# Kernel optimization log

Hardware: AMD Instinct MI355X
Metric: run time of the kernel (lower is better)

The kernel has to match this reference:

```python
import jax, jax.numpy as jnp
import numpy as np
from functools import partial

B, L, V = 64, 512, 20000
P, M = 150, 6          # total patterns, max pattern length
NEG = -1e9             # semiring zero (log-space)
END_STATES = np.repeat(np.array([3, 4, 5]), 50)  # pattern_len-1 per pattern


@jax.custom_vjp
def ste_heaviside(x):
    return (x > 0).astype(x.dtype)

def _ste_fwd(x):
    return ste_heaviside(x), None

def _ste_bwd(_, g):
    return (g,)  # straight-through identity (matches torch code path)

ste_heaviside.defvjp(_ste_fwd, _ste_bwd)


def setup_inputs() -> dict:
    key = jax.random.key(0)
    ks = jax.random.split(key, 8)
    return {
        "docs": jax.random.randint(ks[0], (B, L), 0, V),
        "doc_lens": jax.random.randint(ks[1], (B,), 1, L),
        "local_embeddings": jax.random.normal(ks[2], (300, V), jnp.float32),
        "diags": jax.random.normal(ks[3], (P * M, 300), jnp.float32) * 0.05,
        "bias": jax.random.normal(ks[4], (P * M, 1), jnp.float32) * 0.05,
        "wildcards": jax.random.normal(ks[5], (P, M - 1), jnp.float32) * 0.05,
        "ln_gamma": jnp.ones((P,), jnp.float32),
        "ln_beta": jnp.zeros((P,), jnp.float32),
        "linear_w": jax.random.normal(ks[6], (2, P), jnp.float32) * 0.05,
        "linear_b": jnp.zeros((2,), jnp.float32),
    }


def reference(docs, doc_lens, local_embeddings, diags, bias, wildcards,
              ln_gamma, ln_beta, linear_w, linear_b):
    end_states = jnp.asarray(END_STATES)                  # [P]
    pat_idx = jnp.arange(P)

    # transition matrices over local vocab, mapped into log-space semiring
    tm_vocab = jax.nn.log_sigmoid((diags @ local_embeddings + bias).T)  # [V, P*M]
    tm = tm_vocab[docs].reshape(B, L, P, M)               # [B,L,P,M]

    # wildcard transitions: semiring.times(one=0, log_sigmoid(wildcards))
    wild = jax.nn.log_sigmoid(wildcards)                  # [P, M-1]

    restart = jnp.zeros((B, P, 1), tm.dtype)              # semiring one
    hid0 = jnp.full((B, P, M), NEG, tm.dtype).at[:, :, 0].set(0.0)
    scores0 = jnp.full((B, P), NEG, tm.dtype)             # semiring zero

    def step(carry, inputs):
        hid, sc = carry
        t, tm_t = inputs                                  # tm_t: [B,P,M]
        main = jnp.concatenate([restart, hid[:, :, :-1] + tm_t[:, :, :-1]], axis=2)
        wildp = jnp.concatenate([restart, hid[:, :, :-1] + wild[None]], axis=2)
        hid = jnp.maximum(main, wildp)                    # semiring plus
        esv = hid[:, pat_idx, end_states]                 # [B,P]
        active = (doc_lens > t)[:, None]
        sc = jnp.where(active, jnp.maximum(sc, esv), sc)
        return (hid, sc), None

    xs = (jnp.arange(L), jnp.moveaxis(tm, 1, 0))          # [L], [L,B,P,M]
    (_, scores), _ = jax.lax.scan(step, (hid0, scores0), xs)

    scores = jnp.exp(scores)                              # from_semiring_to_outer
    mu = scores.mean(axis=-1, keepdims=True)
    var = scores.var(axis=-1, keepdims=True)
    norm = (scores - mu) * jax.lax.rsqrt(var + 1e-5) * ln_gamma + ln_beta
    binar = ste_heaviside(norm)
    return binar @ linear_w.T + linear_b
```

## Files before the change

kernel.cpp:

```cpp
#include <hip/hip_runtime.h>
#include <hip/hip_bf16.h>
#include <hip/hip_fp16.h>
#include <math.h>

#define B_   64
#define L_   512
#define V_   20000
#define P_   150
#define M_   6
#define KDIM 300
#define NOUT 750
#define CWS  752
#define NEGF (-1.0e9f)

#define BM 128
#define BN 128
#define BK 16
#define LDP 132

#define KP 320
#define NIT 10
#define NVG 157
#define NJ  6
#define TILE_U4 1024
#define SA 1024.0f
#define SB 16384.0f
#define INV24 (5.9604644775390625e-8f)

#define TCHUNK 32
#define NCHUNK (L_ / TCHUNK)
#define WARM   5
#define CS_STRIDE 160

typedef _Float16 f16x8 __attribute__((ext_vector_type(8)));
typedef float f32x16 __attribute__((ext_vector_type(16)));

__device__ __forceinline__ float logsigf(float x) {
    return fminf(x, 0.f) - log1pf(expf(-fabsf(x)));
}

__device__ __forceinline__ float logsigf_fast(float x) {
    return fminf(x, 0.f) - __logf(1.f + __expf(-fabsf(x)));
}


__global__ __launch_bounds__(256) void p12_split(
    const float* __restrict__ emb, const float* __restrict__ diags,
    uint4* __restrict__ a_t, uint4* __restrict__ b_t)
{
    __shared__ float T[64][132];
    const int t   = threadIdx.x;
    const int bid = blockIdx.x;

    if (bid < NVG * 5) {
        const int gx = bid % NVG;
        const int ky = bid / NVG;
        const int v0 = gx * 128;
        const int k0 = ky * 64;

        #pragma unroll
        for (int pass = 0; pass < 8; ++pass) {
            int flat = pass * 256 + t;
            int krow = flat >> 5;
            int c4   = (flat & 31) * 4;
            int kg   = k0 + krow;
            int v    = v0 + c4;
            float4 f = {0.f, 0.f, 0.f, 0.f};
            if (kg < KDIM && v + 3 < V_)
                f = *(const float4*)(emb + (size_t)kg * V_ + v);
            *(float4*)&T[krow][c4] = f;
        }
        __syncthreads();

        const int vv = t >> 1;
        const int kh = (t & 1) * 32;
        const int it = ky * 2 + (kh >> 5);
        const int v  = v0 + vv;
        if (v < V_) {
            union { ushort u[8]; uint4 q; } H[4], Lo[4];
            #pragma unroll
            for (int i = 0; i < 32; ++i) {
                float x = T[kh + i][vv] * SA;
                __half h = __float2half_rn(x);
                float rem = x - __half2float(h);
                H[i >> 3].u[i & 7]  = __half_as_ushort(h);
                Lo[i >> 3].u[i & 7] = __half_as_ushort(__float2half_rn(rem));
            }
            uint4* tile = a_t + ((size_t)gx * NIT + it) * TILE_U4;
            #pragma unroll
            for (int c = 0; c < 4; ++c) {
                tile[      c * 128 + vv] = H[c].q;
                tile[512 + c * 128 + vv] = Lo[c].q;
            }
        }
    } else {
        const int bidx = bid - NVG * 5;
        const int it   = bidx % NIT;
        const int j    = bidx / NIT;
        const int row  = t >> 1;
        const int qh   = (t & 1) * 2;
        const int n    = j * 128 + row;
        const bool nok = (n < NOUT);
        const int pm   = nok ? ((n / 5) * 6 + (n % 5)) : 0;
        uint4* tile = b_t + (size_t)bidx * TILE_U4;
        #pragma unroll
        for (int qq = 0; qq < 2; ++qq) {
            int q = qh + qq;
            union { ushort u[8]; uint4 v; } H, Lo;
            #pragma unroll
            for (int e = 0; e < 8; ++e) {
                int k = it * 32 + q * 8 + e;
                float x = (nok && k < KDIM) ? diags[(size_t)pm * KDIM + k] * SB : 0.f;
                __half h = __float2half_rn(x);
                float rem = x - __half2float(h);
                H.u[e]  = __half_as_ushort(h);
                Lo.u[e] = __half_as_ushort(__float2half_rn(rem));
            }
            tile[      q * 128 + row] = H.v;
            tile[512 + q * 128 + row] = Lo.v;
        }
    }
}

__global__ __attribute__((amdgpu_waves_per_eu(4))) __launch_bounds__(256)
void k1m_gemm(
    const uint4* __restrict__ a_t, const uint4* __restrict__ b_t,
    const float* __restrict__ bias, const float* __restrict__ wildc,
    float* __restrict__ cw)
{
    const int bid  = blockIdx.x;
    const int xcd  = bid & 7;
    const int slot = bid >> 3;
    const int g    = xcd + 8 * (slot / 6);
    const int j    = slot % 6;
    if (g >= NVG) return;

    const int t    = threadIdx.x;
    const int lane = t & 63;
    const int w    = t >> 6;
    const int wr   = w >> 1, wc = w & 1;
    const int v0   = g * 128;
    const int n0   = j * 128;

    const int fk16 = lane >> 5;
    const int fm   = lane & 31;

    const uint4* abase = a_t + (size_t)g * NIT * TILE_U4;
    const uint4* bbase = b_t + (size_t)j * NIT * TILE_U4;

    f32x16 acc[2][2];
    #pragma unroll
    for (int i = 0; i < 2; ++i)
        #pragma unroll
        for (int jj = 0; jj < 2; ++jj)
            #pragma unroll
            for (int e = 0; e < 16; ++e) acc[i][jj][e] = 0.f;

    #pragma unroll
    for (int it = 0; it < NIT; ++it) {
        const uint4* atile = abase + (size_t)it * TILE_U4;
        const uint4* btile = bbase + (size_t)it * TILE_U4;
        #pragma unroll
        for (int s = 0; s < 2; ++s) {
            const int q = s * 2 + fk16;
            f16x8 A1[2], A2[2], B1[2], B2[2];
            #pragma unroll
            for (int ri = 0; ri < 2; ++ri) {
                const uint4* ap = atile + q * 128 + wr * 64 + ri * 32 + fm;
                A1[ri] = *(const f16x8*)ap;
                A2[ri] = *(const f16x8*)(ap + 512);
            }
            #pragma unroll
            for (int cj = 0; cj < 2; ++cj) {
                const uint4* bp = btile + q * 128 + wc * 64 + cj * 32 + fm;
                B1[cj] = *(const f16x8*)bp;
                B2[cj] = *(const f16x8*)(bp + 512);
            }
            #pragma unroll
            for (int ri = 0; ri < 2; ++ri)
                #pragma unroll
                for (int cj = 0; cj < 2; ++cj) {
                    acc[ri][cj] = __builtin_amdgcn_mfma_f32_32x32x16_f16(A1[ri], B1[cj], acc[ri][cj], 0, 0, 0);
                    acc[ri][cj] = __builtin_amdgcn_mfma_f32_32x32x16_f16(A1[ri], B2[cj], acc[ri][cj], 0, 0, 0);
                    acc[ri][cj] = __builtin_amdgcn_mfma_f32_32x32x16_f16(A2[ri], B1[cj], acc[ri][cj], 0, 0, 0);
                }
        }
    }

    float biasv[2], lwv[2]; int ncol[2]; bool nok[2];
    #pragma unroll
    for (int cj = 0; cj < 2; ++cj) {
        int n = n0 + wc * 64 + cj * 32 + fm;
        ncol[cj] = n;
        nok[cj]  = (n < NOUT);
        int nc = nok[cj] ? n : 0;
        int pm = (nc / 5) * 6 + (nc % 5);
        biasv[cj] = bias[pm];
        lwv[cj]   = logsigf_fast(wildc[nc]);
    }
    #pragma unroll
    for (int ri = 0; ri < 2; ++ri) {
        int vbase = v0 + wr * 64 + ri * 32 + 4 * fk16;
        #pragma unroll
        for (int cj = 0; cj < 2; ++cj) {
            if (!nok[cj]) continue;
            #pragma unroll
            for (int e = 0; e < 16; ++e) {
                int v = vbase + (e & 3) + 8 * (e >> 2);
                if (v < V_) {
                    float val = acc[ri][cj][e] * INV24 + biasv[cj];
                    cw[(size_t)v * CWS + ncol[cj]] = fmaxf(logsigf_fast(val), lwv[cj]);
                }
            }
        }
    }
}


__global__ __launch_bounds__(256) void k1_gemm_cw(
    const float* __restrict__ emb,
    const float* __restrict__ diags,
    const float* __restrict__ bias,
    const float* __restrict__ wildc,
    float* __restrict__ cw)
{
    __shared__ float As[BK][LDP];
    __shared__ float Bs[BK][LDP];

    const int tid = threadIdx.x;
    const int v0 = blockIdx.x * BM;
    const int n0 = blockIdx.y * BN;
    const int tx = tid & 15;
    const int ty = tid >> 4;

    float acc[8][8];
    #pragma unroll
    for (int i = 0; i < 8; ++i)
        #pragma unroll
        for (int j = 0; j < 8; ++j) acc[i][j] = 0.f;

    const int a_k = tid >> 4;
    const int a_v = (tid & 15) * 8;
    const int b_n   = tid >> 1;
    const int b_kof = (tid & 1) * 8;

    int  brow;
    bool bval;
    {
        int n = n0 + b_n;
        bval = (n < NOUT);
        brow = bval ? ((n / 5) * 6 + (n % 5)) : 0;
    }

    for (int k0 = 0; k0 < KDIM; k0 += BK) {
        {
            float4 f0 = {0,0,0,0}, f1 = {0,0,0,0};
            int k = k0 + a_k;
            if (k < KDIM) {
                const float* src = emb + (size_t)k * V_ + v0 + a_v;
                if (v0 + a_v + 3 < V_) f0 = *(const float4*)src;
                if (v0 + a_v + 7 < V_) f1 = *(const float4*)(src + 4);
            }
            *(float4*)&As[a_k][a_v]     = f0;
            *(float4*)&As[a_k][a_v + 4] = f1;
        }
        {
            float4 f = {0,0,0,0}, g = {0,0,0,0};
            if (bval) {
                const float* src = diags + (size_t)brow * KDIM + k0 + b_kof;
                if (k0 + b_kof + 3 < KDIM) f = *(const float4*)src;
                if (k0 + b_kof + 7 < KDIM) g = *(const float4*)(src + 4);
            }
            Bs[b_kof + 0][b_n] = f.x;
            Bs[b_kof + 1][b_n] = f.y;
            Bs[b_kof + 2][b_n] = f.z;
            Bs[b_kof + 3][b_n] = f.w;
            Bs[b_kof + 4][b_n] = g.x;
            Bs[b_kof + 5][b_n] = g.y;
            Bs[b_kof + 6][b_n] = g.z;
            Bs[b_kof + 7][b_n] = g.w;
        }
        __syncthreads();
        #pragma unroll
        for (int k = 0; k < BK; ++k) {
            float4 a0 = *(const float4*)&As[k][tx * 4];
            float4 a1 = *(const float4*)&As[k][64 + tx * 4];
            float4 b0 = *(const float4*)&Bs[k][ty * 8];
            float4 b1 = *(const float4*)&Bs[k][ty * 8 + 4];
            float av[8] = {a0.x, a0.y, a0.z, a0.w, a1.x, a1.y, a1.z, a1.w};
            float bv[8] = {b0.x, b0.y, b0.z, b0.w, b1.x, b1.y, b1.z, b1.w};
            #pragma unroll
            for (int i = 0; i < 8; ++i)
                #pragma unroll
                for (int j = 0; j < 8; ++j)
                    acc[i][j] = fmaf(av[i], bv[j], acc[i][j]);
        }
        __syncthreads();
    }

    float biasv[8], lwv[8];
    #pragma unroll
    for (int j = 0; j < 8; ++j) {
        int n  = n0 + ty * 8 + j;
        int nc = (n < NOUT) ? n : 0;
        int pm = (nc / 5) * 6 + (nc % 5);
        biasv[j] = bias[pm];
        lwv[j]   = logsigf(wildc[nc]);
    }
    #pragma unroll
    for (int i = 0; i < 8; ++i) {
        int v = v0 + ((i < 4) ? (tx * 4 + i) : (64 + tx * 4 + (i - 4)));
        if (v >= V_) continue;
        float r[8];
        #pragma unroll
        for (int j = 0; j < 8; ++j)
            r[j] = fmaxf(logsigf(acc[i][j] + biasv[j]), lwv[j]);
        float* dst = cw + (size_t)v * CWS + n0 + ty * 8;
        if (n0 + ty * 8     < NOUT) *(float4*)dst       = make_float4(r[0], r[1], r[2], r[3]);
        if (n0 + ty * 8 + 4 < NOUT) *(float4*)(dst + 4) = make_float4(r[4], r[5], r[6], r[7]);
    }
}


__global__ __launch_bounds__(192) void k2_scan(
    const int* __restrict__ docs,
    const int* __restrict__ doc_lens,
    const float* __restrict__ cw,
    float* __restrict__ cs)
{
    const int ci = blockIdx.x;
    const int b  = blockIdx.y;
    const int t0 = ci * TCHUNK;
    const int ts = (t0 >= WARM) ? (t0 - WARM) : 0;
    const int dl = doc_lens[b];
    const int te = min(t0 + TCHUNK, dl);
    const int nt = te - ts;

    __shared__ int toks[TCHUNK + WARM];

    const int t = threadIdx.x;
    if (t < TCHUNK + WARM) {
        int tt = ts + t;
        toks[t] = docs[b * L_ + min(tt, L_ - 1)];
    }
    __syncthreads();

    const int p      = t;
    const int e      = (p < 50) ? 3 : (p < 100) ? 4 : 5;
    const int warm_n = t0 - ts;
    float h1 = NEGF, h2 = NEGF, h3 = NEGF, h4 = NEGF, h5 = NEGF, sc = NEGF;

    if (p < P_ && nt > 0) {
        const size_t poff = (size_t)p * 5;
        float A0 = 0, A1 = 0, A2 = 0, A3 = 0, A4 = 0;
        float B0 = 0, B1 = 0, B2 = 0, B3 = 0, B4 = 0;
        {
            const float* r = cw + (size_t)toks[0] * CWS + poff;
            A0 = r[0]; A1 = r[1]; A2 = r[2]; A3 = r[3]; A4 = r[4];
        }
        if (nt > 1) {
            const float* r = cw + (size_t)toks[1] * CWS + poff;
            B0 = r[0]; B1 = r[1]; B2 = r[2]; B3 = r[3]; B4 = r[4];
        }
        for (int i = 0; i < nt; i += 2) {
            float c0 = A0, c1 = A1, c2 = A2, c3 = A3, c4 = A4;
            if (i + 2 < nt) {
                const float* r = cw + (size_t)toks[i + 2] * CWS + poff;
                A0 = r[0]; A1 = r[1]; A2 = r[2]; A3 = r[3]; A4 = r[4];
            }
            h5 = h4 + c4;
            h4 = h3 + c3;
            h3 = h2 + c2;
            h2 = h1 + c1;
            h1 = c0;
            if (i >= warm_n) {
                float esv = (e == 3) ? h3 : (e == 4) ? h4 : h5;
                sc = fmaxf(sc, esv);
            }
            if (i + 1 < nt) {
                float d0 = B0, d1 = B1, d2 = B2, d3 = B3, d4 = B4;
                if (i + 3 < nt) {
                    const float* r = cw + (size_t)toks[i + 3] * CWS + poff;
                    B0 = r[0]; B1 = r[1]; B2 = r[2]; B3 = r[3]; B4 = r[4];
                }
                h5 = h4 + d4;
                h4 = h3 + d3;
                h3 = h2 + d2;
                h2 = h1 + d1;
                h1 = d0;
                if (i + 1 >= warm_n) {
                    float esv = (e == 3) ? h3 : (e == 4) ? h4 : h5;
                    sc = fmaxf(sc, esv);
                }
            }
        }
    }
    if (p < P_) cs[(size_t)(b * NCHUNK + ci) * CS_STRIDE + p] = sc;
}

__device__ __forceinline__ float block_sum192(float v, volatile float* red, int tid) {
    #pragma unroll
    for (int off = 32; off > 0; off >>= 1) v += __shfl_down(v, off, 64);
    __syncthreads();
    if ((tid & 63) == 0) red[tid >> 6] = v;
    __syncthreads();
    return red[0] + red[1] + red[2];
}

__global__ __launch_bounds__(192) void k3_final(
    const float* __restrict__ cs,
    const float* __restrict__ gamma,
    const float* __restrict__ beta,
    const float* __restrict__ lw,
    const float* __restrict__ lb,
    float* __restrict__ out)
{
    __shared__ float red[3];
    const int b   = blockIdx.x;
    const int tid = threadIdx.x;
    float s = 0.f;
    if (tid < P_) {
        float m = NEGF;
        const float* row = cs + (size_t)b * NCHUNK * CS_STRIDE + tid;
        #pragma unroll
        for (int ci = 0; ci < NCHUNK; ++ci) m = fmaxf(m, row[ci * CS_STRIDE]);
        s = expf(m);
    }
    float mu = block_sum192(s, red, tid) * (1.f / P_);
    float d  = (tid < P_) ? (s - mu) : 0.f;
    float var = block_sum192(d * d, red, tid) * (1.f / P_);
    float bin = 0.f;
    if (tid < P_) {
        float norm = (s - mu) * rsqrtf(var + 1e-5f) * gamma[tid] + beta[tid];
        bin = (norm > 0.f) ? 1.f : 0.f;
    }
    float o0 = block_sum192((tid < P_) ? bin * lw[tid]      : 0.f, red, tid);
    float o1 = block_sum192((tid < P_) ? bin * lw[P_ + tid] : 0.f, red, tid);
    if (tid == 0) {
        out[b * 2 + 0] = o0 + lb[0];
        out[b * 2 + 1] = o1 + lb[1];
    }
}

extern "C" void kernel_launch(void* const* d_in, const int* in_sizes, int n_in,
                              void* d_out, int out_size, void* d_ws, size_t ws_size,
                              hipStream_t stream)
{
    const int*   docs  = (const int*)  d_in[0];
    const int*   dlens = (const int*)  d_in[1];
    const float* emb   = (const float*)d_in[2];
    const float* diags = (const float*)d_in[3];
    const float* bias  = (const float*)d_in[4];
    const float* wildc = (const float*)d_in[5];
    const float* gamma = (const float*)d_in[6];
    const float* beta  = (const float*)d_in[7];
    const float* lw    = (const float*)d_in[8];
    const float* lb    = (const float*)d_in[9];
    float* out = (float*)d_out;

    const size_t cw_b = (size_t)V_ * CWS * 4;
    const size_t cs_b = (size_t)B_ * NCHUNK * CS_STRIDE * 4;
    const size_t at_b = (size_t)NVG * NIT * TILE_U4 * 16;
    const size_t bt_b = (size_t)NJ  * NIT * TILE_U4 * 16;
    const size_t need = cw_b + cs_b + at_b + bt_b;

    char* base = (char*)d_ws;
    float* cw = (float*)base;
    float* cs = (float*)(base + cw_b);
    uint4* at = (uint4*)(base + cw_b + cs_b);
    uint4* bt = (uint4*)(base + cw_b + cs_b + at_b);

    if (ws_size >= need) {
        p12_split<<<NVG * 5 + NJ * NIT, 256, 0, stream>>>(emb, diags, at, bt);
        k1m_gemm<<<960, 256, 0, stream>>>(at, bt, bias, wildc, cw);
    } else {
        dim3 g1((V_ + BM - 1) / BM, (NOUT + BN - 1) / BN);
        k1_gemm_cw<<<g1, 256, 0, stream>>>(emb, diags, bias, wildc, cw);
    }

    dim3 g2(NCHUNK, B_);
    k2_scan<<<g2, 192, 0, stream>>>(docs, dlens, cw, cs);
    k3_final<<<B_, 192, 0, stream>>>(cs, gamma, beta, lw, lb, out);
}
```

Before: 158.8 us.

## Enlarge GEMM block and warp tiles to raise register reuse of operands

The split-fp16 MFMA GEMM now uses 512-thread blocks covering 256 vocab rows by 256 output columns. Each wave computes a 128x64 tile with 4x2 accumulators instead of 64x64, and the grid drops from 960 to 240 blocks with a new block-to-XCD mapping. Each wave gets more MFMAs per global fragment load, which cuts redundant global and cache traffic. In exchange it needs far more accumulator registers, runs at 2 waves per EU, and the last row group is clamped so it recomputes and rewrites identical values.

After: 156.8 us. About the same (-1.2%).

```diff
diff --git a/kernel.cpp b/kernel.cpp
--- a/kernel.cpp
+++ b/kernel.cpp
@@ -122,35 +122,36 @@
     }
 }
 
-__global__ __attribute__((amdgpu_waves_per_eu(4))) __launch_bounds__(256)
+__global__ __attribute__((amdgpu_waves_per_eu(2, 2))) __launch_bounds__(512)
 void k1m_gemm(
     const uint4* __restrict__ a_t, const uint4* __restrict__ b_t,
     const float* __restrict__ bias, const float* __restrict__ wildc,
     float* __restrict__ cw)
 {
-    const int bid  = blockIdx.x;
-    const int xcd  = bid & 7;
-    const int slot = bid >> 3;
-    const int g    = xcd + 8 * (slot / 6);
-    const int j    = slot % 6;
-    if (g >= NVG) return;
+    const int bid = blockIdx.x;
+    const int c   = bid / 24;
+    const int r   = bid % 24;
+    const int gp  = c * 8 + (r & 7);
+    const int h   = r >> 3;
+    if (gp >= 79) return;
 
     const int t    = threadIdx.x;
     const int lane = t & 63;
     const int w    = t >> 6;
-    const int wr   = w >> 1, wc = w & 1;
-    const int v0   = g * 128;
-    const int n0   = j * 128;
-
+    const int wr   = w >> 2;
+    const int wc   = w & 3;
     const int fk16 = lane >> 5;
     const int fm   = lane & 31;
 
-    const uint4* abase = a_t + (size_t)g * NIT * TILE_U4;
-    const uint4* bbase = b_t + (size_t)j * NIT * TILE_U4;
-
-    f32x16 acc[2][2];
-    #pragma unroll
-    for (int i = 0; i < 2; ++i)
+    const int ga = (2 * gp + wr < NVG) ? (2 * gp + wr) : (NVG - 1);
+    const uint4* abase = a_t + (size_t)ga * NIT * TILE_U4;
+    const int bg   = 2 * h + (wc >> 1);
+    const int bcol = (wc & 1) * 64;
+    const uint4* bbase = b_t + (size_t)bg * NIT * TILE_U4;
+
+    f32x16 acc[4][2];
+    #pragma unroll
+    for (int i = 0; i < 4; ++i)
         #pragma unroll
         for (int jj = 0; jj < 2; ++jj)
             #pragma unroll
@@ -163,21 +164,21 @@
         #pragma unroll
         for (int s = 0; s < 2; ++s) {
             const int q = s * 2 + fk16;
-            f16x8 A1[2], A2[2], B1[2], B2[2];
-            #pragma unroll
-            for (int ri = 0; ri < 2; ++ri) {
-                const uint4* ap = atile + q * 128 + wr * 64 + ri * 32 + fm;
+            f16x8 A1[4], A2[4], B1[2], B2[2];
+            #pragma unroll
+            for (int ri = 0; ri < 4; ++ri) {
+                const uint4* ap = atile + q * 128 + ri * 32 + fm;
                 A1[ri] = *(const f16x8*)ap;
                 A2[ri] = *(const f16x8*)(ap + 512);
             }
             #pragma unroll
             for (int cj = 0; cj < 2; ++cj) {
-                const uint4* bp = btile + q * 128 + wc * 64 + cj * 32 + fm;
+                const uint4* bp = btile + q * 128 + bcol + cj * 32 + fm;
                 B1[cj] = *(const f16x8*)bp;
                 B2[cj] = *(const f16x8*)(bp + 512);
             }
             #pragma unroll
-            for (int ri = 0; ri < 2; ++ri)
+            for (int ri = 0; ri < 4; ++ri)
                 #pragma unroll
                 for (int cj = 0; cj < 2; ++cj) {
                     acc[ri][cj] = __builtin_amdgcn_mfma_f32_32x32x16_f16(A1[ri], B1[cj], acc[ri][cj], 0, 0, 0);
@@ -190,7 +191,7 @@
     float biasv[2], lwv[2]; int ncol[2]; bool nok[2];
     #pragma unroll
     for (int cj = 0; cj < 2; ++cj) {
-        int n = n0 + wc * 64 + cj * 32 + fm;
+        int n = h * 256 + wc * 64 + cj * 32 + fm;
         ncol[cj] = n;
         nok[cj]  = (n < NOUT);
         int nc = nok[cj] ? n : 0;
@@ -198,9 +199,10 @@
         biasv[cj] = bias[pm];
         lwv[cj]   = logsigf_fast(wildc[nc]);
     }
-    #pragma unroll
-    for (int ri = 0; ri < 2; ++ri) {
-        int vbase = v0 + wr * 64 + ri * 32 + 4 * fk16;
+    const int v0 = ga * 128;
+    #pragma unroll
+    for (int ri = 0; ri < 4; ++ri) {
+        int vbase = v0 + ri * 32 + 4 * fk16;
         #pragma unroll
         for (int cj = 0; cj < 2; ++cj) {
             if (!nok[cj]) continue;
@@ -472,7 +474,7 @@
 
     if (ws_size >= need) {
         p12_split<<<NVG * 5 + NJ * NIT, 256, 0, stream>>>(emb, diags, at, bt);
-        k1m_gemm<<<960, 256, 0, stream>>>(at, bt, bias, wildc, cw);
+        k1m_gemm<<<240, 512, 0, stream>>>(at, bt, bias, wildc, cw);
     } else {
         dim3 g1((V_ + BM - 1) / BM, (NOUT + BN - 1) / BN);
         k1_gemm_cw<<<g1, 256, 0, stream>>>(emb, diags, bias, wildc, cw);
```
